# Kernel optimization log

Hardware: AMD Instinct MI355X
Metric: run time of the kernel (lower is better)

The kernel has to match this reference:

```python
import jax, jax.numpy as jnp
import numpy as np

EPS = 1e-5

def _layer_norm(x, gamma, beta):
    m = jnp.mean(x, axis=-1, keepdims=True)
    v = jnp.mean(jnp.square(x - m), axis=-1, keepdims=True)
    return (x - m) * jax.lax.rsqrt(v + EPS) * gamma + beta

def setup_inputs() -> dict:
    key = jax.random.key(0)
    ks = jax.random.split(key, 6)
    B, D, H = 4096, 1024, 1024
    s = 1.0 / np.sqrt(H)
    return {
        "inputs": jax.random.normal(ks[0], (B, D), jnp.float32),
        "hx": jax.random.normal(ks[1], (B, H), jnp.float32),
        "cx": jax.random.normal(ks[2], (B, H), jnp.float32),
        "w_ih": jax.random.uniform(ks[3], (4 * H, D), jnp.float32, -s, s),
        "w_hh": jax.random.uniform(ks[4], (4 * H, H), jnp.float32, -s, s),
        "b_hh": jax.random.uniform(ks[5], (4 * H,), jnp.float32, -s, s),
        "g_ih": jnp.ones((4 * H,), jnp.float32),
        "beta_ih": jnp.zeros((4 * H,), jnp.float32),
        "g_hh": jnp.ones((4 * H,), jnp.float32),
        "beta_hh": jnp.zeros((4 * H,), jnp.float32),
        "g_ho": jnp.ones((H,), jnp.float32),
        "beta_ho": jnp.zeros((H,), jnp.float32),
    }

def reference(inputs, hx, cx, w_ih, w_hh, b_hh, g_ih, beta_ih, g_hh, beta_hh, g_ho, beta_ho):
    # i2h: [B, 4H] (no input bias used in original forward)
    i2h = inputs @ w_ih.T
    h2h = hx @ w_hh.T + b_hh
    gates = _layer_norm(i2h, g_ih, beta_ih) + _layer_norm(h2h, g_hh, beta_hh)
    i, f, o, g = jnp.split(gates, 4, axis=1)  # torch chunk order: i, f, o, g
    cy = jax.nn.sigmoid(f) * cx + jax.nn.sigmoid(i) * jnp.tanh(g)
    hy = jax.nn.sigmoid(o) * _layer_norm(jnp.tanh(cy), g_ho, beta_ho)
    # Dropout(0.1) is identity in eval / deterministic reference
    return hy, cy
```

## Files before the change

kernel.cpp:

```cpp
#include <hip/hip_runtime.h>
#include <hip/hip_bf16.h>
#include <stdint.h>

typedef __attribute__((ext_vector_type(8))) short bf16x8;
typedef __attribute__((ext_vector_type(4))) float f32x4;

#define LN_EPS 1e-5f

__device__ inline unsigned short f2bf(float f) {
    unsigned u = __builtin_bit_cast(unsigned, f);
    u += 0x7fffu + ((u >> 16) & 1u);
    return (unsigned short)(u >> 16);
}
__device__ inline float bf2f(unsigned short u) {
    return __builtin_bit_cast(float, ((unsigned)u) << 16);
}
__device__ inline float sigf(float x) {
    return 1.0f / (1.0f + __expf(-x));
}
__device__ inline float tanh_fast(float x) {
    return __builtin_fmaf(2.0f, 1.0f / (1.0f + __expf(-2.0f * x)), -1.0f);
}
__device__ inline float wred(float v) {
#pragma unroll
    for (int o = 32; o > 0; o >>= 1) v += __shfl_xor(v, o);
    return v;
}
__device__ inline void gload_lds16(const void* g, void* l) {
    __builtin_amdgcn_global_load_lds(
        (const __attribute__((address_space(1))) void*)g,
        (__attribute__((address_space(3))) void*)l, 16, 0, 0);
}

__global__ __launch_bounds__(256) void cast_kernel(const float4* __restrict__ src,
                                                   ushort4* __restrict__ dst, int n4) {
    int i = blockIdx.x * blockDim.x + threadIdx.x;
    if (i < n4) {
        float4 v = src[i];
        ushort4 o;
        o.x = f2bf(v.x); o.y = f2bf(v.y); o.z = f2bf(v.z); o.w = f2bf(v.w);
        dst[i] = o;
    }
}

#define GNT 32

__global__ __launch_bounds__(512) void gemm8p(
    const short* __restrict__ Aa, const short* __restrict__ Ba, unsigned short* __restrict__ Ca,
    const short* __restrict__ Ab, const short* __restrict__ Bb, unsigned short* __restrict__ Cb,
    const float* __restrict__ Bias,
    float2* __restrict__ P,
    int N, int K)
{
    __shared__ __attribute__((aligned(16))) short lds[65536];
    short* ldsA = lds;
    short* ldsB = lds + 32768;

    const int gx  = gridDim.x;
    const int gxy = gx * gridDim.y;
    int bid = (blockIdx.z * gridDim.y + blockIdx.y) * gx + blockIdx.x;
    const int cpx = (gxy * gridDim.z) >> 3;
    int swz = (bid & 7) * cpx + (bid >> 3);
    const int z  = swz / gxy;
    const int r2 = swz - z * gxy;
    const int by = r2 / gx;
    const int bx = r2 - by * gx;

    const short* __restrict__ A = z ? Ab : Aa;
    const short* __restrict__ B = z ? Bb : Ba;
    unsigned short* __restrict__ C = z ? Cb : Ca;
    const int brow = by * 256, bcol = bx * 256;

    const int t    = threadIdx.x;
    const int lane = t & 63, w = t >> 6;
    const int wr = w >> 2, wc = w & 3;
    const int lr = lane & 15, kc = lane >> 4;

    const int ci0 = t, ci1 = t + 512;
    const int r0 = ci0 >> 2, l0 = (ci0 & 3) ^ ((r0 >> 1) & 3);
    const int r1 = ci1 >> 2, l1 = (ci1 & 3) ^ ((r1 >> 1) & 3);
    const int gA0 = (brow + r0) * K + l0 * 8;
    const int gA1 = (brow + r1) * K + l1 * 8;
    const int gB0 = (bcol + r0) * K + l0 * 8;
    const int gB1 = (bcol + r1) * K + l1 * 8;
    const int d0 = ci0 * 8, d1 = ci1 * 8;

#define STAGE_A(u) { const int so_ = ((u) & 3) * 8192; \
    gload_lds16(A + gA0 + (u) * 32, ldsA + so_ + d0);  \
    gload_lds16(A + gA1 + (u) * 32, ldsA + so_ + d1); }
#define STAGE_B(u) { const int so_ = ((u) & 3) * 8192; \
    gload_lds16(B + gB0 + (u) * 32, ldsB + so_ + d0);  \
    gload_lds16(B + gB1 + (u) * 32, ldsB + so_ + d1); }

    int offA[8], offBn[4];
#pragma unroll
    for (int f = 0; f < 8; ++f) {
        int r = wr * 128 + f * 16 + lr;
        offA[f] = r * 32 + ((kc ^ ((r >> 1) & 3)) * 8);
    }
#pragma unroll
    for (int n = 0; n < 4; ++n) {
        int r = wc * 64 + n * 16 + lr;
        offBn[n] = r * 32 + ((kc ^ ((r >> 1) & 3)) * 8);
    }

    f32x4 acc[8][4];
#pragma unroll
    for (int i = 0; i < 8; ++i)
#pragma unroll
        for (int j = 0; j < 4; ++j)
            acc[i][j] = (f32x4){0.f, 0.f, 0.f, 0.f};

    STAGE_A(0); STAGE_B(0); STAGE_A(1); STAGE_B(1); STAGE_A(2);
    asm volatile("s_waitcnt vmcnt(6)" ::: "memory");
    __builtin_amdgcn_s_barrier();

#pragma unroll 4
    for (int T = 0; T < GNT; ++T) {
        const int so = (T & 3) * 8192;
        bf16x8 a0, a1, a2, a3, b0, b1, b2, b3;

        a0 = *(const bf16x8*)&ldsA[so + offA[0]];
        a1 = *(const bf16x8*)&ldsA[so + offA[1]];
        a2 = *(const bf16x8*)&ldsA[so + offA[2]];
        a3 = *(const bf16x8*)&ldsA[so + offA[3]];
        b0 = *(const bf16x8*)&ldsB[so + offBn[0]];
        b1 = *(const bf16x8*)&ldsB[so + offBn[1]];
        b2 = *(const bf16x8*)&ldsB[so + offBn[2]];
        b3 = *(const bf16x8*)&ldsB[so + offBn[3]];
        if (T + 2 < GNT) STAGE_B(T + 2);
        __builtin_amdgcn_s_barrier();
        asm volatile("s_waitcnt lgkmcnt(0)" ::: "memory");
        __builtin_amdgcn_sched_barrier(0);
        __builtin_amdgcn_s_setprio(1);
        acc[0][0] = __builtin_amdgcn_mfma_f32_16x16x32_bf16(a0, b0, acc[0][0], 0, 0, 0);
        acc[0][1] = __builtin_amdgcn_mfma_f32_16x16x32_bf16(a0, b1, acc[0][1], 0, 0, 0);
        acc[0][2] = __builtin_amdgcn_mfma_f32_16x16x32_bf16(a0, b2, acc[0][2], 0, 0, 0);
        acc[0][3] = __builtin_amdgcn_mfma_f32_16x16x32_bf16(a0, b3, acc[0][3], 0, 0, 0);
        acc[1][0] = __builtin_amdgcn_mfma_f32_16x16x32_bf16(a1, b0, acc[1][0], 0, 0, 0);
        acc[1][1] = __builtin_amdgcn_mfma_f32_16x16x32_bf16(a1, b1, acc[1][1], 0, 0, 0);
        acc[1][2] = __builtin_amdgcn_mfma_f32_16x16x32_bf16(a1, b2, acc[1][2], 0, 0, 0);
        acc[1][3] = __builtin_amdgcn_mfma_f32_16x16x32_bf16(a1, b3, acc[1][3], 0, 0, 0);
        acc[2][0] = __builtin_amdgcn_mfma_f32_16x16x32_bf16(a2, b0, acc[2][0], 0, 0, 0);
        acc[2][1] = __builtin_amdgcn_mfma_f32_16x16x32_bf16(a2, b1, acc[2][1], 0, 0, 0);
        acc[2][2] = __builtin_amdgcn_mfma_f32_16x16x32_bf16(a2, b2, acc[2][2], 0, 0, 0);
        acc[2][3] = __builtin_amdgcn_mfma_f32_16x16x32_bf16(a2, b3, acc[2][3], 0, 0, 0);
        acc[3][0] = __builtin_amdgcn_mfma_f32_16x16x32_bf16(a3, b0, acc[3][0], 0, 0, 0);
        acc[3][1] = __builtin_amdgcn_mfma_f32_16x16x32_bf16(a3, b1, acc[3][1], 0, 0, 0);
        acc[3][2] = __builtin_amdgcn_mfma_f32_16x16x32_bf16(a3, b2, acc[3][2], 0, 0, 0);
        acc[3][3] = __builtin_amdgcn_mfma_f32_16x16x32_bf16(a3, b3, acc[3][3], 0, 0, 0);
        __builtin_amdgcn_s_setprio(0);
        __builtin_amdgcn_s_barrier();

        a0 = *(const bf16x8*)&ldsA[so + offA[4]];
        a1 = *(const bf16x8*)&ldsA[so + offA[5]];
        a2 = *(const bf16x8*)&ldsA[so + offA[6]];
        a3 = *(const bf16x8*)&ldsA[so + offA[7]];
        if (T + 3 < GNT) STAGE_A(T + 3);
        __builtin_amdgcn_s_barrier();
        asm volatile("s_waitcnt lgkmcnt(0)" ::: "memory");
        __builtin_amdgcn_sched_barrier(0);
        __builtin_amdgcn_s_setprio(1);
        acc[4][0] = __builtin_amdgcn_mfma_f32_16x16x32_bf16(a0, b0, acc[4][0], 0, 0, 0);
        acc[4][1] = __builtin_amdgcn_mfma_f32_16x16x32_bf16(a0, b1, acc[4][1], 0, 0, 0);
        acc[4][2] = __builtin_amdgcn_mfma_f32_16x16x32_bf16(a0, b2, acc[4][2], 0, 0, 0);
        acc[4][3] = __builtin_amdgcn_mfma_f32_16x16x32_bf16(a0, b3, acc[4][3], 0, 0, 0);
        acc[5][0] = __builtin_amdgcn_mfma_f32_16x16x32_bf16(a1, b0, acc[5][0], 0, 0, 0);
        acc[5][1] = __builtin_amdgcn_mfma_f32_16x16x32_bf16(a1, b1, acc[5][1], 0, 0, 0);
        acc[5][2] = __builtin_amdgcn_mfma_f32_16x16x32_bf16(a1, b2, acc[5][2], 0, 0, 0);
        acc[5][3] = __builtin_amdgcn_mfma_f32_16x16x32_bf16(a1, b3, acc[5][3], 0, 0, 0);
        acc[6][0] = __builtin_amdgcn_mfma_f32_16x16x32_bf16(a2, b0, acc[6][0], 0, 0, 0);
        acc[6][1] = __builtin_amdgcn_mfma_f32_16x16x32_bf16(a2, b1, acc[6][1], 0, 0, 0);
        acc[6][2] = __builtin_amdgcn_mfma_f32_16x16x32_bf16(a2, b2, acc[6][2], 0, 0, 0);
        acc[6][3] = __builtin_amdgcn_mfma_f32_16x16x32_bf16(a2, b3, acc[6][3], 0, 0, 0);
        acc[7][0] = __builtin_amdgcn_mfma_f32_16x16x32_bf16(a3, b0, acc[7][0], 0, 0, 0);
        acc[7][1] = __builtin_amdgcn_mfma_f32_16x16x32_bf16(a3, b1, acc[7][1], 0, 0, 0);
        acc[7][2] = __builtin_amdgcn_mfma_f32_16x16x32_bf16(a3, b2, acc[7][2], 0, 0, 0);
        acc[7][3] = __builtin_amdgcn_mfma_f32_16x16x32_bf16(a3, b3, acc[7][3], 0, 0, 0);
        __builtin_amdgcn_s_setprio(0);
        if (T < GNT - 3)      { asm volatile("s_waitcnt vmcnt(6)" ::: "memory"); }
        else if (T == GNT - 3){ asm volatile("s_waitcnt vmcnt(4)" ::: "memory"); }
        else if (T == GNT - 2){ asm volatile("s_waitcnt vmcnt(0)" ::: "memory"); }
        __builtin_amdgcn_s_barrier();
    }

    const int crow = wr * 128 + kc * 4;
    const int ccol = wc * 64 + lr;
    float bias[4];
#pragma unroll
    for (int in = 0; in < 4; ++in)
        bias[in] = z ? Bias[bcol + ccol + in * 16] : 0.f;

    __syncthreads();
    float2* part = (float2*)lds;

#pragma unroll
    for (int ai = 0; ai < 8; ++ai) {
        float rs[4] = {0.f, 0.f, 0.f, 0.f};
        float rq[4] = {0.f, 0.f, 0.f, 0.f};
#pragma unroll
        for (int in = 0; in < 4; ++in) {
#pragma unroll
            for (int r = 0; r < 4; ++r) {
                float v = acc[ai][in][r] + bias[in];
                unsigned short us = f2bf(v);
                float vf = bf2f(us);
                C[(size_t)(brow + crow + ai * 16 + r) * N + bcol + ccol + in * 16] = us;
                rs[r] += vf; rq[r] += vf * vf;
            }
        }
#pragma unroll
        for (int r = 0; r < 4; ++r) {
            float s = rs[r], q = rq[r];
#pragma unroll
            for (int o = 8; o > 0; o >>= 1) { s += __shfl_xor(s, o); q += __shfl_xor(q, o); }
            if (lr == 0) {
                float2 pr; pr.x = s; pr.y = q;
                part[wc * 256 + crow + ai * 16 + r] = pr;
            }
        }
    }
    __syncthreads();
    if (t < 256) {
        float2 a0 = part[t], a1 = part[256 + t], a2 = part[512 + t], a3 = part[768 + t];
        float2 o; o.x = a0.x + a1.x + a2.x + a3.x; o.y = a0.y + a1.y + a2.y + a3.y;
        P[((size_t)(z * 16 + by) * 256 + t) * 16 + bx] = o;
    }
#undef STAGE_A
#undef STAGE_B
}

__global__ __launch_bounds__(256) void reduce_stats(const float2* __restrict__ P,
                                                    float2* __restrict__ stats, float invn) {
    const int row = blockIdx.x * 256 + threadIdx.x;
    float s = 0.f, q = 0.f;
#pragma unroll
    for (int b = 0; b < 16; ++b) { float2 v = P[(size_t)row * 16 + b]; s += v.x; q += v.y; }
    float m = s * invn;
    float r = rsqrtf(q * invn - m * m + LN_EPS);
    float2 o; o.x = m; o.y = r;
    stats[row] = o;
}

__global__ __launch_bounds__(256) void ln_lstm(
    const unsigned short* __restrict__ i2h,
    const unsigned short* __restrict__ h2h,
    const float* __restrict__ cx,
    const float2* __restrict__ statsI, const float2* __restrict__ statsH,
    const float* __restrict__ g_ih, const float* __restrict__ be_ih,
    const float* __restrict__ g_hh, const float* __restrict__ be_hh,
    const float* __restrict__ g_ho, const float* __restrict__ be_ho,
    float* __restrict__ hy, float* __restrict__ cy, int H)
{
    const int b = blockIdx.x;
    const int t = threadIdx.x;
    const int lane = t & 63;
    const int wave = t >> 6;
    const int H4 = 4 * H;
    const int h0 = t * 4;

    const unsigned short* xi = i2h + (size_t)b * H4;
    const unsigned short* xh = h2h + (size_t)b * H4;

    const float2 sI = statsI[b];
    const float2 sH = statsH[b];

    __shared__ float red[4][2];

    float gate[4][4];
#pragma unroll
    for (int q = 0; q < 4; ++q) {
        const int j = q * H + h0;
        ushort4 vi = *reinterpret_cast<const ushort4*>(&xi[j]);
        ushort4 vh = *reinterpret_cast<const ushort4*>(&xh[j]);
        float4 gi = *reinterpret_cast<const float4*>(&g_ih[j]);
        float4 bi = *reinterpret_cast<const float4*>(&be_ih[j]);
        float4 gh = *reinterpret_cast<const float4*>(&g_hh[j]);
        float4 bh = *reinterpret_cast<const float4*>(&be_hh[j]);
        gate[q][0] = (bf2f(vi.x) - sI.x) * sI.y * gi.x + bi.x + (bf2f(vh.x) - sH.x) * sH.y * gh.x + bh.x;
        gate[q][1] = (bf2f(vi.y) - sI.x) * sI.y * gi.y + bi.y + (bf2f(vh.y) - sH.x) * sH.y * gh.y + bh.y;
        gate[q][2] = (bf2f(vi.z) - sI.x) * sI.y * gi.z + bi.z + (bf2f(vh.z) - sH.x) * sH.y * gh.z + bh.z;
        gate[q][3] = (bf2f(vi.w) - sI.x) * sI.y * gi.w + bi.w + (bf2f(vh.w) - sH.x) * sH.y * gh.w + bh.w;
    }

    float4 cxv = *reinterpret_cast<const float4*>(&cx[(size_t)b * H + h0]);
    float cvals[4] = {cxv.x, cxv.y, cxv.z, cxv.w};
    float tv[4], ov[4];
    float s2 = 0.f, q2 = 0.f;
    float4 cyv;
#pragma unroll
    for (int k = 0; k < 4; ++k) {
        float c = sigf(gate[1][k]) * cvals[k] + sigf(gate[0][k]) * tanh_fast(gate[3][k]);
        ((float*)&cyv)[k] = c;
        float tc = tanh_fast(c);
        tv[k] = tc; ov[k] = sigf(gate[2][k]);
        s2 += tc; q2 += tc * tc;
    }
    *reinterpret_cast<float4*>(&cy[(size_t)b * H + h0]) = cyv;

    s2 = wred(s2); q2 = wred(q2);
    if (lane == 0) { red[wave][0] = s2; red[wave][1] = q2; }
    __syncthreads();
    float S2 = red[0][0] + red[1][0] + red[2][0] + red[3][0];
    float Q2 = red[0][1] + red[1][1] + red[2][1] + red[3][1];
    const float invH = 1.0f / (float)H;
    float mt = S2 * invH;
    float rt = rsqrtf(Q2 * invH - mt * mt + LN_EPS);

    float4 go = *reinterpret_cast<const float4*>(&g_ho[h0]);
    float4 bo = *reinterpret_cast<const float4*>(&be_ho[h0]);
    float4 hyv;
    hyv.x = ov[0] * ((tv[0] - mt) * rt * go.x + bo.x);
    hyv.y = ov[1] * ((tv[1] - mt) * rt * go.y + bo.y);
    hyv.z = ov[2] * ((tv[2] - mt) * rt * go.z + bo.z);
    hyv.w = ov[3] * ((tv[3] - mt) * rt * go.w + bo.w);
    *reinterpret_cast<float4*>(&hy[(size_t)b * H + h0]) = hyv;
}

extern "C" void kernel_launch(void* const* d_in, const int* in_sizes, int n_in,
                              void* d_out, int out_size, void* d_ws, size_t ws_size,
                              hipStream_t stream) {
    const float* inputs  = (const float*)d_in[0];
    const float* hx      = (const float*)d_in[1];
    const float* cx      = (const float*)d_in[2];
    const float* w_ih    = (const float*)d_in[3];
    const float* w_hh    = (const float*)d_in[4];
    const float* b_hh    = (const float*)d_in[5];
    const float* g_ih    = (const float*)d_in[6];
    const float* beta_ih = (const float*)d_in[7];
    const float* g_hh    = (const float*)d_in[8];
    const float* beta_hh = (const float*)d_in[9];
    const float* g_ho    = (const float*)d_in[10];
    const float* beta_ho = (const float*)d_in[11];

    const int H  = in_sizes[10];
    const int B  = in_sizes[1] / H;
    const int D  = in_sizes[0] / B;
    const int H4 = 4 * H;

    uint8_t* ws = (uint8_t*)d_ws;
    size_t off = 0;
    short* Abf  = (short*)(ws + off); off += (size_t)B * D * 2;
    short* Hbf  = (short*)(ws + off); off += (size_t)B * H * 2;
    short* Wih  = (short*)(ws + off); off += (size_t)H4 * D * 2;
    short* Whh  = (short*)(ws + off); off += (size_t)H4 * H * 2;
    unsigned short* i2hb = (unsigned short*)(ws + off); off += (size_t)B * H4 * 2;
    unsigned short* h2hb = (unsigned short*)(ws + off); off += (size_t)B * H4 * 2;
    float2* P     = (float2*)(ws + off); off += (size_t)2 * 16 * 256 * 16 * sizeof(float2);
    float2* stats = (float2*)(ws + off); off += (size_t)2 * B * sizeof(float2);

    float* hy  = (float*)d_out;
    float* cyo = (float*)d_out + (size_t)B * H;

    {
        int n4 = (B * D) / 4;
        cast_kernel<<<(n4 + 255) / 256, 256, 0, stream>>>((const float4*)inputs, (ushort4*)Abf, n4);
        n4 = (B * H) / 4;
        cast_kernel<<<(n4 + 255) / 256, 256, 0, stream>>>((const float4*)hx, (ushort4*)Hbf, n4);
        n4 = (H4 * D) / 4;
        cast_kernel<<<(n4 + 255) / 256, 256, 0, stream>>>((const float4*)w_ih, (ushort4*)Wih, n4);
        n4 = (H4 * H) / 4;
        cast_kernel<<<(n4 + 255) / 256, 256, 0, stream>>>((const float4*)w_hh, (ushort4*)Whh, n4);
    }

    {
        dim3 grid(H4 / 256, B / 256, 2);
        gemm8p<<<grid, 512, 0, stream>>>(Abf, Wih, i2hb, Hbf, Whh, h2hb, b_hh, P, H4, D);
    }

    reduce_stats<<<(2 * B) / 256, 256, 0, stream>>>(P, stats, 1.0f / (float)H4);

    ln_lstm<<<B, 256, 0, stream>>>(i2hb, h2hb, cx, stats, stats + B,
                                   g_ih, beta_ih, g_hh, beta_hh, g_ho, beta_ho,
                                   hy, cyo, H);
}
```

Before: 136.6 us.

## Swap GEMM operand roles for packed bf16 stores and merge cast launches

Swaps which LDS tile feeds each MFMA operand, so each lane's four accumulator values lie along contiguous output columns. The epilogue can then pack four bf16 values into one 8-byte store and reduce row statistics with fewer shuffles and fewer LDS partials. Replacing 2-byte scattered stores should cut store-instruction overhead in the GEMM epilogue. The four fp32-to-bf16 cast launches are also merged into one kernel to save launch overhead, at the cost of per-thread branching to pick the source buffer.

```diff
diff --git a/kernel.cpp b/kernel.cpp
--- a/kernel.cpp
+++ b/kernel.cpp
@@ -7,13 +7,13 @@
 
 #define LN_EPS 1e-5f
 
-__device__ inline unsigned short f2bf(float f) {
+__device__ inline unsigned f2bf(float f) {
     unsigned u = __builtin_bit_cast(unsigned, f);
     u += 0x7fffu + ((u >> 16) & 1u);
-    return (unsigned short)(u >> 16);
-}
-__device__ inline float bf2f(unsigned short u) {
-    return __builtin_bit_cast(float, ((unsigned)u) << 16);
+    return u >> 16;
+}
+__device__ inline float bf2f(unsigned u) {
+    return __builtin_bit_cast(float, u << 16);
 }
 __device__ inline float sigf(float x) {
     return 1.0f / (1.0f + __expf(-x));
@@ -32,15 +32,33 @@
         (__attribute__((address_space(3))) void*)l, 16, 0, 0);
 }
 
-__global__ __launch_bounds__(256) void cast_kernel(const float4* __restrict__ src,
-                                                   ushort4* __restrict__ dst, int n4) {
-    int i = blockIdx.x * blockDim.x + threadIdx.x;
-    if (i < n4) {
-        float4 v = src[i];
-        ushort4 o;
-        o.x = f2bf(v.x); o.y = f2bf(v.y); o.z = f2bf(v.z); o.w = f2bf(v.w);
-        dst[i] = o;
-    }
+__global__ __launch_bounds__(256) void cast_all(
+    const float4* __restrict__ s0, ushort4* __restrict__ d0, int n0,
+    const float4* __restrict__ s1, ushort4* __restrict__ d1, int n1,
+    const float4* __restrict__ s2, ushort4* __restrict__ d2, int n2,
+    const float4* __restrict__ s3, ushort4* __restrict__ d3, int n3)
+{
+    int j = blockIdx.x * blockDim.x + threadIdx.x;
+    const float4* s; ushort4* d;
+    if (j < n0) { s = s0; d = d0; }
+    else {
+        j -= n0;
+        if (j < n1) { s = s1; d = d1; }
+        else {
+            j -= n1;
+            if (j < n2) { s = s2; d = d2; }
+            else {
+                j -= n2;
+                if (j >= n3) return;
+                s = s3; d = d3;
+            }
+        }
+    }
+    float4 v = s[j];
+    ushort4 o;
+    o.x = (unsigned short)f2bf(v.x); o.y = (unsigned short)f2bf(v.y);
+    o.z = (unsigned short)f2bf(v.z); o.w = (unsigned short)f2bf(v.w);
+    d[j] = o;
 }
 
 #define GNT 32
@@ -92,16 +110,16 @@
     gload_lds16(B + gB0 + (u) * 32, ldsB + so_ + d0);  \
     gload_lds16(B + gB1 + (u) * 32, ldsB + so_ + d1); }
 
-    int offA[8], offBn[4];
+    int offW[8], offX[4];
 #pragma unroll
     for (int f = 0; f < 8; ++f) {
         int r = wr * 128 + f * 16 + lr;
-        offA[f] = r * 32 + ((kc ^ ((r >> 1) & 3)) * 8);
+        offW[f] = r * 32 + ((kc ^ ((r >> 1) & 3)) * 8);
     }
 #pragma unroll
     for (int n = 0; n < 4; ++n) {
         int r = wc * 64 + n * 16 + lr;
-        offBn[n] = r * 32 + ((kc ^ ((r >> 1) & 3)) * 8);
+        offX[n] = r * 32 + ((kc ^ ((r >> 1) & 3)) * 8);
     }
 
     f32x4 acc[8][4];
@@ -118,65 +136,65 @@
 #pragma unroll 4
     for (int T = 0; T < GNT; ++T) {
         const int so = (T & 3) * 8192;
-        bf16x8 a0, a1, a2, a3, b0, b1, b2, b3;
-
-        a0 = *(const bf16x8*)&ldsA[so + offA[0]];
-        a1 = *(const bf16x8*)&ldsA[so + offA[1]];
-        a2 = *(const bf16x8*)&ldsA[so + offA[2]];
-        a3 = *(const bf16x8*)&ldsA[so + offA[3]];
-        b0 = *(const bf16x8*)&ldsB[so + offBn[0]];
-        b1 = *(const bf16x8*)&ldsB[so + offBn[1]];
-        b2 = *(const bf16x8*)&ldsB[so + offBn[2]];
-        b3 = *(const bf16x8*)&ldsB[so + offBn[3]];
+        bf16x8 w0, w1, w2, w3, x0, x1, x2, x3;
+
+        w0 = *(const bf16x8*)&ldsB[so + offW[0]];
+        w1 = *(const bf16x8*)&ldsB[so + offW[1]];
+        w2 = *(const bf16x8*)&ldsB[so + offW[2]];
+        w3 = *(const bf16x8*)&ldsB[so + offW[3]];
+        x0 = *(const bf16x8*)&ldsA[so + offX[0]];
+        x1 = *(const bf16x8*)&ldsA[so + offX[1]];
+        x2 = *(const bf16x8*)&ldsA[so + offX[2]];
+        x3 = *(const bf16x8*)&ldsA[so + offX[3]];
         if (T + 2 < GNT) STAGE_B(T + 2);
         __builtin_amdgcn_s_barrier();
         asm volatile("s_waitcnt lgkmcnt(0)" ::: "memory");
         __builtin_amdgcn_sched_barrier(0);
         __builtin_amdgcn_s_setprio(1);
-        acc[0][0] = __builtin_amdgcn_mfma_f32_16x16x32_bf16(a0, b0, acc[0][0], 0, 0, 0);
-        acc[0][1] = __builtin_amdgcn_mfma_f32_16x16x32_bf16(a0, b1, acc[0][1], 0, 0, 0);
-        acc[0][2] = __builtin_amdgcn_mfma_f32_16x16x32_bf16(a0, b2, acc[0][2], 0, 0, 0);
-        acc[0][3] = __builtin_amdgcn_mfma_f32_16x16x32_bf16(a0, b3, acc[0][3], 0, 0, 0);
-        acc[1][0] = __builtin_amdgcn_mfma_f32_16x16x32_bf16(a1, b0, acc[1][0], 0, 0, 0);
-        acc[1][1] = __builtin_amdgcn_mfma_f32_16x16x32_bf16(a1, b1, acc[1][1], 0, 0, 0);
-        acc[1][2] = __builtin_amdgcn_mfma_f32_16x16x32_bf16(a1, b2, acc[1][2], 0, 0, 0);
-        acc[1][3] = __builtin_amdgcn_mfma_f32_16x16x32_bf16(a1, b3, acc[1][3], 0, 0, 0);
-        acc[2][0] = __builtin_amdgcn_mfma_f32_16x16x32_bf16(a2, b0, acc[2][0], 0, 0, 0);
-        acc[2][1] = __builtin_amdgcn_mfma_f32_16x16x32_bf16(a2, b1, acc[2][1], 0, 0, 0);
-        acc[2][2] = __builtin_amdgcn_mfma_f32_16x16x32_bf16(a2, b2, acc[2][2], 0, 0, 0);
-        acc[2][3] = __builtin_amdgcn_mfma_f32_16x16x32_bf16(a2, b3, acc[2][3], 0, 0, 0);
-        acc[3][0] = __builtin_amdgcn_mfma_f32_16x16x32_bf16(a3, b0, acc[3][0], 0, 0, 0);
-        acc[3][1] = __builtin_amdgcn_mfma_f32_16x16x32_bf16(a3, b1, acc[3][1], 0, 0, 0);
-        acc[3][2] = __builtin_amdgcn_mfma_f32_16x16x32_bf16(a3, b2, acc[3][2], 0, 0, 0);
-        acc[3][3] = __builtin_amdgcn_mfma_f32_16x16x32_bf16(a3, b3, acc[3][3], 0, 0, 0);
+        acc[0][0] = __builtin_amdgcn_mfma_f32_16x16x32_bf16(w0, x0, acc[0][0], 0, 0, 0);
+        acc[0][1] = __builtin_amdgcn_mfma_f32_16x16x32_bf16(w0, x1, acc[0][1], 0, 0, 0);
+        acc[0][2] = __builtin_amdgcn_mfma_f32_16x16x32_bf16(w0, x2, acc[0][2], 0, 0, 0);
+        acc[0][3] = __builtin_amdgcn_mfma_f32_16x16x32_bf16(w0, x3, acc[0][3], 0, 0, 0);
+        acc[1][0] = __builtin_amdgcn_mfma_f32_16x16x32_bf16(w1, x0, acc[1][0], 0, 0, 0);
+        acc[1][1] = __builtin_amdgcn_mfma_f32_16x16x32_bf16(w1, x1, acc[1][1], 0, 0, 0);
+        acc[1][2] = __builtin_amdgcn_mfma_f32_16x16x32_bf16(w1, x2, acc[1][2], 0, 0, 0);
+        acc[1][3] = __builtin_amdgcn_mfma_f32_16x16x32_bf16(w1, x3, acc[1][3], 0, 0, 0);
+        acc[2][0] = __builtin_amdgcn_mfma_f32_16x16x32_bf16(w2, x0, acc[2][0], 0, 0, 0);
+        acc[2][1] = __builtin_amdgcn_mfma_f32_16x16x32_bf16(w2, x1, acc[2][1], 0, 0, 0);
+        acc[2][2] = __builtin_amdgcn_mfma_f32_16x16x32_bf16(w2, x2, acc[2][2], 0, 0, 0);
+        acc[2][3] = __builtin_amdgcn_mfma_f32_16x16x32_bf16(w2, x3, acc[2][3], 0, 0, 0);
+        acc[3][0] = __builtin_amdgcn_mfma_f32_16x16x32_bf16(w3, x0, acc[3][0], 0, 0, 0);
+        acc[3][1] = __builtin_amdgcn_mfma_f32_16x16x32_bf16(w3, x1, acc[3][1], 0, 0, 0);
+        acc[3][2] = __builtin_amdgcn_mfma_f32_16x16x32_bf16(w3, x2, acc[3][2], 0, 0, 0);
+        acc[3][3] = __builtin_amdgcn_mfma_f32_16x16x32_bf16(w3, x3, acc[3][3], 0, 0, 0);
         __builtin_amdgcn_s_setprio(0);
         __builtin_amdgcn_s_barrier();
 
-        a0 = *(const bf16x8*)&ldsA[so + offA[4]];
-        a1 = *(const bf16x8*)&ldsA[so + offA[5]];
-        a2 = *(const bf16x8*)&ldsA[so + offA[6]];
-        a3 = *(const bf16x8*)&ldsA[so + offA[7]];
+        w0 = *(const bf16x8*)&ldsB[so + offW[4]];
+        w1 = *(const bf16x8*)&ldsB[so + offW[5]];
+        w2 = *(const bf16x8*)&ldsB[so + offW[6]];
+        w3 = *(const bf16x8*)&ldsB[so + offW[7]];
         if (T + 3 < GNT) STAGE_A(T + 3);
         __builtin_amdgcn_s_barrier();
         asm volatile("s_waitcnt lgkmcnt(0)" ::: "memory");
         __builtin_amdgcn_sched_barrier(0);
         __builtin_amdgcn_s_setprio(1);
-        acc[4][0] = __builtin_amdgcn_mfma_f32_16x16x32_bf16(a0, b0, acc[4][0], 0, 0, 0);
-        acc[4][1] = __builtin_amdgcn_mfma_f32_16x16x32_bf16(a0, b1, acc[4][1], 0, 0, 0);
-        acc[4][2] = __builtin_amdgcn_mfma_f32_16x16x32_bf16(a0, b2, acc[4][2], 0, 0, 0);
-        acc[4][3] = __builtin_amdgcn_mfma_f32_16x16x32_bf16(a0, b3, acc[4][3], 0, 0, 0);
-        acc[5][0] = __builtin_amdgcn_mfma_f32_16x16x32_bf16(a1, b0, acc[5][0], 0, 0, 0);
-        acc[5][1] = __builtin_amdgcn_mfma_f32_16x16x32_bf16(a1, b1, acc[5][1], 0, 0, 0);
-        acc[5][2] = __builtin_amdgcn_mfma_f32_16x16x32_bf16(a1, b2, acc[5][2], 0, 0, 0);
-        acc[5][3] = __builtin_amdgcn_mfma_f32_16x16x32_bf16(a1, b3, acc[5][3], 0, 0, 0);
-        acc[6][0] = __builtin_amdgcn_mfma_f32_16x16x32_bf16(a2, b0, acc[6][0], 0, 0, 0);
-        acc[6][1] = __builtin_amdgcn_mfma_f32_16x16x32_bf16(a2, b1, acc[6][1], 0, 0, 0);
-        acc[6][2] = __builtin_amdgcn_mfma_f32_16x16x32_bf16(a2, b2, acc[6][2], 0, 0, 0);
-        acc[6][3] = __builtin_amdgcn_mfma_f32_16x16x32_bf16(a2, b3, acc[6][3], 0, 0, 0);
-        acc[7][0] = __builtin_amdgcn_mfma_f32_16x16x32_bf16(a3, b0, acc[7][0], 0, 0, 0);
-        acc[7][1] = __builtin_amdgcn_mfma_f32_16x16x32_bf16(a3, b1, acc[7][1], 0, 0, 0);
-        acc[7][2] = __builtin_amdgcn_mfma_f32_16x16x32_bf16(a3, b2, acc[7][2], 0, 0, 0);
-        acc[7][3] = __builtin_amdgcn_mfma_f32_16x16x32_bf16(a3, b3, acc[7][3], 0, 0, 0);
+        acc[4][0] = __builtin_amdgcn_mfma_f32_16x16x32_bf16(w0, x0, acc[4][0], 0, 0, 0);
+        acc[4][1] = __builtin_amdgcn_mfma_f32_16x16x32_bf16(w0, x1, acc[4][1], 0, 0, 0);
+        acc[4][2] = __builtin_amdgcn_mfma_f32_16x16x32_bf16(w0, x2, acc[4][2], 0, 0, 0);
+        acc[4][3] = __builtin_amdgcn_mfma_f32_16x16x32_bf16(w0, x3, acc[4][3], 0, 0, 0);
+        acc[5][0] = __builtin_amdgcn_mfma_f32_16x16x32_bf16(w1, x0, acc[5][0], 0, 0, 0);
+        acc[5][1] = __builtin_amdgcn_mfma_f32_16x16x32_bf16(w1, x1, acc[5][1], 0, 0, 0);
+        acc[5][2] = __builtin_amdgcn_mfma_f32_16x16x32_bf16(w1, x2, acc[5][2], 0, 0, 0);
+        acc[5][3] = __builtin_amdgcn_mfma_f32_16x16x32_bf16(w1, x3, acc[5][3], 0, 0, 0);
+        acc[6][0] = __builtin_amdgcn_mfma_f32_16x16x32_bf16(w2, x0, acc[6][0], 0, 0, 0);
+        acc[6][1] = __builtin_amdgcn_mfma_f32_16x16x32_bf16(w2, x1, acc[6][1], 0, 0, 0);
+        acc[6][2] = __builtin_amdgcn_mfma_f32_16x16x32_bf16(w2, x2, acc[6][2], 0, 0, 0);
+        acc[6][3] = __builtin_amdgcn_mfma_f32_16x16x32_bf16(w2, x3, acc[6][3], 0, 0, 0);
+        acc[7][0] = __builtin_amdgcn_mfma_f32_16x16x32_bf16(w3, x0, acc[7][0], 0, 0, 0);
+        acc[7][1] = __builtin_amdgcn_mfma_f32_16x16x32_bf16(w3, x1, acc[7][1], 0, 0, 0);
+        acc[7][2] = __builtin_amdgcn_mfma_f32_16x16x32_bf16(w3, x2, acc[7][2], 0, 0, 0);
+        acc[7][3] = __builtin_amdgcn_mfma_f32_16x16x32_bf16(w3, x3, acc[7][3], 0, 0, 0);
         __builtin_amdgcn_s_setprio(0);
         if (T < GNT - 3)      { asm volatile("s_waitcnt vmcnt(6)" ::: "memory"); }
         else if (T == GNT - 3){ asm volatile("s_waitcnt vmcnt(4)" ::: "memory"); }
@@ -184,46 +202,52 @@
         __builtin_amdgcn_s_barrier();
     }
 
-    const int crow = wr * 128 + kc * 4;
-    const int ccol = wc * 64 + lr;
-    float bias[4];
-#pragma unroll
-    for (int in = 0; in < 4; ++in)
-        bias[in] = z ? Bias[bcol + ccol + in * 16] : 0.f;
+    const int gc0   = bcol + wr * 128 + kc * 4;
+    const int mrow0 = brow + wc * 64 + lr;
+
+    float4 bias4[8];
+#pragma unroll
+    for (int f = 0; f < 8; ++f) {
+        if (z) bias4[f] = *reinterpret_cast<const float4*>(&Bias[gc0 + f * 16]);
+        else   bias4[f] = (float4){0.f, 0.f, 0.f, 0.f};
+    }
+
+    float s[4] = {0.f, 0.f, 0.f, 0.f}, q[4] = {0.f, 0.f, 0.f, 0.f};
+#pragma unroll
+    for (int f = 0; f < 8; ++f) {
+#pragma unroll
+        for (int n = 0; n < 4; ++n) {
+            float v0 = acc[f][n][0] + bias4[f].x;
+            float v1 = acc[f][n][1] + bias4[f].y;
+            float v2 = acc[f][n][2] + bias4[f].z;
+            float v3 = acc[f][n][3] + bias4[f].w;
+            unsigned u0 = f2bf(v0), u1 = f2bf(v1), u2 = f2bf(v2), u3 = f2bf(v3);
+            float e0 = bf2f(u0), e1 = bf2f(u1), e2 = bf2f(u2), e3 = bf2f(u3);
+            s[n] += (e0 + e1) + (e2 + e3);
+            q[n] += (e0 * e0 + e1 * e1) + (e2 * e2 + e3 * e3);
+            uint2 pk; pk.x = u0 | (u1 << 16); pk.y = u2 | (u3 << 16);
+            *reinterpret_cast<uint2*>(&C[(size_t)(mrow0 + n * 16) * N + gc0 + f * 16]) = pk;
+        }
+    }
+#pragma unroll
+    for (int n = 0; n < 4; ++n) {
+        s[n] += __shfl_xor(s[n], 16); s[n] += __shfl_xor(s[n], 32);
+        q[n] += __shfl_xor(q[n], 16); q[n] += __shfl_xor(q[n], 32);
+    }
 
     __syncthreads();
     float2* part = (float2*)lds;
-
-#pragma unroll
-    for (int ai = 0; ai < 8; ++ai) {
-        float rs[4] = {0.f, 0.f, 0.f, 0.f};
-        float rq[4] = {0.f, 0.f, 0.f, 0.f};
-#pragma unroll
-        for (int in = 0; in < 4; ++in) {
-#pragma unroll
-            for (int r = 0; r < 4; ++r) {
-                float v = acc[ai][in][r] + bias[in];
-                unsigned short us = f2bf(v);
-                float vf = bf2f(us);
-                C[(size_t)(brow + crow + ai * 16 + r) * N + bcol + ccol + in * 16] = us;
-                rs[r] += vf; rq[r] += vf * vf;
-            }
-        }
-#pragma unroll
-        for (int r = 0; r < 4; ++r) {
-            float s = rs[r], q = rq[r];
-#pragma unroll
-            for (int o = 8; o > 0; o >>= 1) { s += __shfl_xor(s, o); q += __shfl_xor(q, o); }
-            if (lr == 0) {
-                float2 pr; pr.x = s; pr.y = q;
-                part[wc * 256 + crow + ai * 16 + r] = pr;
-            }
+    if (kc == 0) {
+#pragma unroll
+        for (int n = 0; n < 4; ++n) {
+            float2 pr; pr.x = s[n]; pr.y = q[n];
+            part[wr * 256 + wc * 64 + n * 16 + lr] = pr;
         }
     }
     __syncthreads();
     if (t < 256) {
-        float2 a0 = part[t], a1 = part[256 + t], a2 = part[512 + t], a3 = part[768 + t];
-        float2 o; o.x = a0.x + a1.x + a2.x + a3.x; o.y = a0.y + a1.y + a2.y + a3.y;
+        float2 p0 = part[t], p1 = part[256 + t];
+        float2 o; o.x = p0.x + p1.x; o.y = p0.y + p1.y;
         P[((size_t)(z * 16 + by) * 256 + t) * 16 + bx] = o;
     }
 #undef STAGE_A
@@ -353,14 +377,13 @@
     float* cyo = (float*)d_out + (size_t)B * H;
 
     {
-        int n4 = (B * D) / 4;
-        cast_kernel<<<(n4 + 255) / 256, 256, 0, stream>>>((const float4*)inputs, (ushort4*)Abf, n4);
-        n4 = (B * H) / 4;
-        cast_kernel<<<(n4 + 255) / 256, 256, 0, stream>>>((const float4*)hx, (ushort4*)Hbf, n4);
-        n4 = (H4 * D) / 4;
-        cast_kernel<<<(n4 + 255) / 256, 256, 0, stream>>>((const float4*)w_ih, (ushort4*)Wih, n4);
-        n4 = (H4 * H) / 4;
-        cast_kernel<<<(n4 + 255) / 256, 256, 0, stream>>>((const float4*)w_hh, (ushort4*)Whh, n4);
+        const int n0 = (B * D) / 4, n1 = (B * H) / 4, n2 = (H4 * D) / 4, n3 = (H4 * H) / 4;
+        const int tot = n0 + n1 + n2 + n3;
+        cast_all<<<(tot + 255) / 256, 256, 0, stream>>>(
+            (const float4*)inputs, (ushort4*)Abf, n0,
+            (const float4*)hx,     (ushort4*)Hbf, n1,
+            (const float4*)w_ih,   (ushort4*)Wih, n2,
+            (const float4*)w_hh,   (ushort4*)Whh, n3);
     }
 
     {
```

After: 127.8 us. 6.5% less time.
